# Optimization experiments

Hardware: AMD Instinct MI355X
Metric: run time of the kernel (lower is better)

The kernel has to match this reference:

```python
import jax, jax.numpy as jnp
import numpy as np

D = 1024
H = 16
DH = D // H
RATIO = 4
EPS = 1e-5


def layer_norm(x, g, b):
    mu = jnp.mean(x, axis=-1, keepdims=True)
    var = jnp.mean(jnp.square(x - mu), axis=-1, keepdims=True)
    return (x - mu) * jax.lax.rsqrt(var + EPS) * g + b


def setup_inputs() -> dict:
    key = jax.random.key(0)
    ks = jax.random.split(key, 12)
    s = 1.0 / np.sqrt(D)
    inp = {
        "x": jax.random.normal(ks[0], (4, 2048, D), dtype=jnp.float32),
        "Wq": jax.random.normal(ks[1], (D, D), dtype=jnp.float32) * s,
        "bq": jnp.zeros((D,), jnp.float32),
        "Wk": jax.random.normal(ks[2], (D, D), dtype=jnp.float32) * s,
        "bk": jnp.zeros((D,), jnp.float32),
        "Wv": jax.random.normal(ks[3], (D, D), dtype=jnp.float32) * s,
        "bv": jnp.zeros((D,), jnp.float32),
        "Wfc": jax.random.normal(ks[4], (D, D), dtype=jnp.float32) * s,
        "bfc": jnp.zeros((D,), jnp.float32),
        "ln1_g": jnp.ones((D,), jnp.float32),
        "ln1_b": jnp.zeros((D,), jnp.float32),
        "W1": jax.random.normal(ks[5], (D, D * RATIO), dtype=jnp.float32) * s,
        "b1": jnp.zeros((D * RATIO,), jnp.float32),
        "W2": jax.random.normal(ks[6], (D * RATIO, D), dtype=jnp.float32) * (1.0 / np.sqrt(D * RATIO)),
        "b2": jnp.zeros((D,), jnp.float32),
        "ln2_g": jnp.ones((D,), jnp.float32),
        "ln2_b": jnp.zeros((D,), jnp.float32),
    }
    return inp


def reference(x, Wq, bq, Wk, bk, Wv, bv, Wfc, bfc, ln1_g, ln1_b, W1, b1, W2, b2, ln2_g, ln2_b):
    B, S, _ = x.shape
    # QKV projections -> [B, H, S, DH]
    q = (x @ Wq + bq).reshape(B, S, H, DH).transpose(0, 2, 1, 3)
    k = (x @ Wk + bk).reshape(B, S, H, DH).transpose(0, 2, 1, 3)
    v = (x @ Wv + bv).reshape(B, S, H, DH).transpose(0, 2, 1, 3)
    scores = jnp.einsum("bhqd,bhkd->bhqk", q, k) / np.sqrt(DH)
    w = jax.nn.softmax(scores, axis=-1)
    attn = jnp.einsum("bhqk,bhkd->bhqd", w, v)
    attn = attn.transpose(0, 2, 1, 3).reshape(B, S, D)
    attn_out = attn @ Wfc + bfc  # dropout = identity (droprate=0)
    h = layer_norm(x + attn_out, ln1_g, ln1_b)
    m = jax.nn.relu(h @ W1 + b1)
    m = m @ W2 + b2
    # NOTE: original code applies mlp_norm without residual
    return layer_norm(m, ln2_g, ln2_b)
```

## Files before the change

### kernel.cpp

```cpp
#include <hip/hip_runtime.h>
#include <hip/hip_bf16.h>

#define DEV __device__ __forceinline__

typedef __attribute__((ext_vector_type(8))) short short8;
typedef __attribute__((ext_vector_type(4))) float f32x4;

DEV f32x4 mfma16(short8 a, short8 b, f32x4 c) {
  return __builtin_amdgcn_mfma_f32_16x16x32_bf16(a, b, c, 0, 0, 0);
}

DEV unsigned short f2bf(float f) {
  union { float f; unsigned u; } x; x.f = f;
  unsigned r = x.u + 0x7fffu + ((x.u >> 16) & 1u);
  return (unsigned short)(r >> 16);
}

__global__ __launch_bounds__(256) void cvt_bf16(const float* __restrict__ in,
                                                unsigned short* __restrict__ out,
                                                int n4) {
  int i = blockIdx.x * 256 + threadIdx.x;
  if (i >= n4) return;
  float4 v = ((const float4*)in)[i];
  ushort4 o;
  o.x = f2bf(v.x); o.y = f2bf(v.y); o.z = f2bf(v.z); o.w = f2bf(v.w);
  ((ushort4*)out)[i] = o;
}

__global__ __launch_bounds__(256) void cvtT(const float* __restrict__ W,
                                            unsigned short* __restrict__ Wt,
                                            int K, int N) {
  __shared__ float t[32][33];
  int n0 = blockIdx.x * 32, k0 = blockIdx.y * 32;
  int tx = threadIdx.x, ty = threadIdx.y;
#pragma unroll
  for (int i = 0; i < 4; i++)
    t[ty * 4 + i][tx] = W[(size_t)(k0 + ty * 4 + i) * N + n0 + tx];
  __syncthreads();
#pragma unroll
  for (int i = 0; i < 4; i++)
    Wt[(size_t)(n0 + ty * 4 + i) * K + k0 + tx] = f2bf(t[tx][ty * 4 + i]);
}

enum { M_Q = 0, M_K = 1, M_V = 2, M_RES = 3, M_RELU = 4, M_F32 = 5 };

template <int MODE>
__global__ __launch_bounds__(256, 2)
void gemm_bt(const unsigned short* __restrict__ A,
             const unsigned short* __restrict__ Bt,
             const float* __restrict__ bias,
             const float* __restrict__ res,
             void* __restrict__ outp, int M, int N, int K) {
  __shared__ unsigned short lA[128 * 64];
  __shared__ unsigned short lB[128 * 64];
  const int tid = threadIdx.x;
  const int l = tid & 63, w = tid >> 6;
  const int wr = w >> 1, wc = w & 1;
  const int lr = l & 15, lg = l >> 4;
  const int m0 = blockIdx.x * 128, n0 = blockIdx.y * 128;
  f32x4 acc[4][4] = {};

  for (int k0 = 0; k0 < K; k0 += 64) {
    __syncthreads();
#pragma unroll
    for (int i = 0; i < 4; i++) {
      int off = (i * 256 + tid) * 8;
      int r = off >> 6, c = off & 63;
      __builtin_amdgcn_global_load_lds(
          (const __attribute__((address_space(1))) unsigned int*)(A + (size_t)(m0 + r) * K + k0 + c),
          (__attribute__((address_space(3))) unsigned int*)(lA + off), 16, 0, 0);
    }
#pragma unroll
    for (int i = 0; i < 4; i++) {
      int off = (i * 256 + tid) * 8;
      int r = off >> 6, c = off & 63;
      __builtin_amdgcn_global_load_lds(
          (const __attribute__((address_space(1))) unsigned int*)(Bt + (size_t)(n0 + r) * K + k0 + c),
          (__attribute__((address_space(3))) unsigned int*)(lB + off), 16, 0, 0);
    }
    __syncthreads();
#pragma unroll
    for (int kk = 0; kk < 2; kk++) {
      short8 af[4], bfr[4];
#pragma unroll
      for (int mt = 0; mt < 4; mt++)
        af[mt] = *(const short8*)(lA + (wr * 64 + mt * 16 + lr) * 64 + kk * 32 + lg * 8);
#pragma unroll
      for (int nt = 0; nt < 4; nt++)
        bfr[nt] = *(const short8*)(lB + (wc * 64 + nt * 16 + lr) * 64 + kk * 32 + lg * 8);
#pragma unroll
      for (int mt = 0; mt < 4; mt++)
#pragma unroll
        for (int nt = 0; nt < 4; nt++)
          acc[mt][nt] = mfma16(af[mt], bfr[nt], acc[mt][nt]);
    }
  }

#pragma unroll
  for (int mt = 0; mt < 4; mt++) {
#pragma unroll
    for (int nt = 0; nt < 4; nt++) {
#pragma unroll
      for (int r = 0; r < 4; r++) {
        int row = m0 + wr * 64 + mt * 16 + lg * 4 + r;
        int col = n0 + wc * 64 + nt * 16 + lr;
        float v = acc[mt][nt][r] + bias[col];
        if constexpr (MODE == M_Q || MODE == M_K || MODE == M_V) {
          int b = row >> 11, s = row & 2047;
          int h = col >> 6, dh = col & 63;
          if constexpr (MODE == M_Q) {
            ((unsigned short*)outp)[(((size_t)(b * 16 + h) * 2048 + s) << 6) + dh] = f2bf(v * 0.125f);
          } else if constexpr (MODE == M_K) {
            ((unsigned short*)outp)[(((size_t)(b * 16 + h) * 2048 + s) << 6) + dh] = f2bf(v);
          } else {
            ((unsigned short*)outp)[((size_t)(b * 16 + h) * 64 + dh) * 2048 + s] = f2bf(v);
          }
        } else if constexpr (MODE == M_RES) {
          size_t idx = (size_t)row * N + col;
          ((float*)outp)[idx] = v + res[idx];
        } else if constexpr (MODE == M_RELU) {
          ((unsigned short*)outp)[(size_t)row * N + col] = f2bf(v > 0.f ? v : 0.f);
        } else {
          ((float*)outp)[(size_t)row * N + col] = v;
        }
      }
    }
  }
}

__global__ __launch_bounds__(256, 2)
void flash_attn(const unsigned short* __restrict__ Q,
                const unsigned short* __restrict__ Kb,
                const unsigned short* __restrict__ Vt,
                unsigned short* __restrict__ attnb) {
  const int S = 2048;
  __shared__ unsigned short Qs[64 * 64], Ks[64 * 64], Vs[64 * 64];
  __shared__ unsigned short Ps[4][16 * 64];
  const int tid = threadIdx.x, l = tid & 63, w = tid >> 6;
  const int lr = l & 15, lg = l >> 4;
  const int bh = blockIdx.y, q0 = blockIdx.x * 64;
  const unsigned short* Qp = Q + (size_t)bh * S * 64;
  const unsigned short* Kp = Kb + (size_t)bh * S * 64;
  const unsigned short* Vp = Vt + (size_t)bh * 64 * S;

#pragma unroll
  for (int i = 0; i < 2; i++) {
    int off = (i * 256 + tid) * 8;
    int r = off >> 6, c = off & 63;
    *(short8*)((char*)Qs + r * 128 + ((c * 2) ^ ((r & 7) << 4))) =
        *(const short8*)(Qp + (size_t)(q0 + r) * 64 + c);
  }
  __syncthreads();
  short8 qf[2];
#pragma unroll
  for (int kk = 0; kk < 2; kk++) {
    int rq = w * 16 + lr;
    qf[kk] = *(const short8*)((char*)Qs + rq * 128 + (((kk * 32 + lg * 8) * 2) ^ ((rq & 7) << 4)));
  }

  float m_run[4], l_run[4];
  f32x4 oacc[4] = {};
#pragma unroll
  for (int r = 0; r < 4; r++) { m_run[r] = -1e30f; l_run[r] = 0.f; }

  for (int kv0 = 0; kv0 < S; kv0 += 64) {
    __syncthreads();
#pragma unroll
    for (int i = 0; i < 2; i++) {
      int off = (i * 256 + tid) * 8;
      int r = off >> 6, c = off & 63;
      *(short8*)((char*)Ks + r * 128 + ((c * 2) ^ ((r & 7) << 4))) =
          *(const short8*)(Kp + (size_t)(kv0 + r) * 64 + c);
      *(short8*)((char*)Vs + r * 128 + ((c * 2) ^ ((r & 7) << 4))) =
          *(const short8*)(Vp + (size_t)r * S + kv0 + c);
    }
    __syncthreads();

    f32x4 sa[4] = {};
#pragma unroll
    for (int nt = 0; nt < 4; nt++) {
#pragma unroll
      for (int kk = 0; kk < 2; kk++) {
        int rk = nt * 16 + lr;
        short8 kf = *(const short8*)((char*)Ks + rk * 128 + (((kk * 32 + lg * 8) * 2) ^ ((rk & 7) << 4)));
        sa[nt] = mfma16(qf[kk], kf, sa[nt]);
      }
    }

    float tmax[4], p[4][4], tsum[4];
#pragma unroll
    for (int r = 0; r < 4; r++)
      tmax[r] = fmaxf(fmaxf(sa[0][r], sa[1][r]), fmaxf(sa[2][r], sa[3][r]));
#pragma unroll
    for (int d = 1; d < 16; d <<= 1)
#pragma unroll
      for (int r = 0; r < 4; r++) tmax[r] = fmaxf(tmax[r], __shfl_xor(tmax[r], d, 64));
#pragma unroll
    for (int r = 0; r < 4; r++) {
      float mnew = fmaxf(m_run[r], tmax[r]);
      float corr = __expf(m_run[r] - mnew);
      tsum[r] = 0.f;
#pragma unroll
      for (int nt = 0; nt < 4; nt++) { p[nt][r] = __expf(sa[nt][r] - mnew); tsum[r] += p[nt][r]; }
      m_run[r] = mnew;
      l_run[r] *= corr;
#pragma unroll
      for (int nt = 0; nt < 4; nt++) oacc[nt][r] *= corr;
    }
#pragma unroll
    for (int d = 1; d < 16; d <<= 1)
#pragma unroll
      for (int r = 0; r < 4; r++) tsum[r] += __shfl_xor(tsum[r], d, 64);
#pragma unroll
    for (int r = 0; r < 4; r++) l_run[r] += tsum[r];

    unsigned short* Pw = Ps[w];
#pragma unroll
    for (int nt = 0; nt < 4; nt++)
#pragma unroll
      for (int r = 0; r < 4; r++) {
        int rr = lg * 4 + r;
        *(unsigned short*)((char*)Pw + rr * 128 + (((nt * 16 + lr) * 2) ^ ((rr & 7) << 4))) = f2bf(p[nt][r]);
      }
#pragma unroll
    for (int kk = 0; kk < 2; kk++) {
      short8 pf = *(const short8*)((char*)Pw + lr * 128 + (((kk * 32 + lg * 8) * 2) ^ ((lr & 7) << 4)));
#pragma unroll
      for (int nt = 0; nt < 4; nt++) {
        int rv = nt * 16 + lr;
        short8 vf = *(const short8*)((char*)Vs + rv * 128 + (((kk * 32 + lg * 8) * 2) ^ ((rv & 7) << 4)));
        oacc[nt] = mfma16(pf, vf, oacc[nt]);
      }
    }
  }

  const int b = bh >> 4, h = bh & 15;
#pragma unroll
  for (int nt = 0; nt < 4; nt++)
#pragma unroll
    for (int r = 0; r < 4; r++) {
      int s = q0 + w * 16 + lg * 4 + r;
      int col = h * 64 + nt * 16 + lr;
      attnb[(size_t)(b * 2048 + s) * 1024 + col] = f2bf(oacc[nt][r] / l_run[r]);
    }
}

template <int OUTF32>
__global__ __launch_bounds__(256)
void ln_row(const float* __restrict__ in, const float* __restrict__ g,
            const float* __restrict__ b, void* __restrict__ outp) {
  const int row = blockIdx.x, tid = threadIdx.x;
  float4 v = ((const float4*)(in + (size_t)row * 1024))[tid];
  float s = v.x + v.y + v.z + v.w;
  float s2 = v.x * v.x + v.y * v.y + v.z * v.z + v.w * v.w;
#pragma unroll
  for (int d = 1; d < 64; d <<= 1) { s += __shfl_xor(s, d, 64); s2 += __shfl_xor(s2, d, 64); }
  __shared__ float ps[8];
  if ((tid & 63) == 0) { ps[tid >> 6] = s; ps[4 + (tid >> 6)] = s2; }
  __syncthreads();
  s = ps[0] + ps[1] + ps[2] + ps[3];
  s2 = ps[4] + ps[5] + ps[6] + ps[7];
  float mu = s * (1.f / 1024.f);
  float var = s2 * (1.f / 1024.f) - mu * mu;
  float rstd = rsqrtf(var + 1e-5f);
  float4 gv = ((const float4*)g)[tid];
  float4 bv = ((const float4*)b)[tid];
  float o0 = (v.x - mu) * rstd * gv.x + bv.x;
  float o1 = (v.y - mu) * rstd * gv.y + bv.y;
  float o2 = (v.z - mu) * rstd * gv.z + bv.z;
  float o3 = (v.w - mu) * rstd * gv.w + bv.w;
  if constexpr (OUTF32) {
    float4 o; o.x = o0; o.y = o1; o.z = o2; o.w = o3;
    ((float4*)outp)[(size_t)row * 256 + tid] = o;
  } else {
    ushort4 o; o.x = f2bf(o0); o.y = f2bf(o1); o.z = f2bf(o2); o.w = f2bf(o3);
    ((ushort4*)outp)[(size_t)row * 256 + tid] = o;
  }
}

extern "C" void kernel_launch(void* const* d_in, const int* in_sizes, int n_in,
                              void* d_out, int out_size, void* d_ws, size_t ws_size,
                              hipStream_t stream) {
  const float* x   = (const float*)d_in[0];
  const float* Wq  = (const float*)d_in[1];
  const float* bq  = (const float*)d_in[2];
  const float* Wk  = (const float*)d_in[3];
  const float* bk  = (const float*)d_in[4];
  const float* Wv  = (const float*)d_in[5];
  const float* bv  = (const float*)d_in[6];
  const float* Wfc = (const float*)d_in[7];
  const float* bfc = (const float*)d_in[8];
  const float* g1  = (const float*)d_in[9];
  const float* bn1 = (const float*)d_in[10];
  const float* W1  = (const float*)d_in[11];
  const float* b1  = (const float*)d_in[12];
  const float* W2  = (const float*)d_in[13];
  const float* b2  = (const float*)d_in[14];
  const float* g2  = (const float*)d_in[15];
  const float* bn2 = (const float*)d_in[16];

  char* ws = (char*)d_ws;
  size_t off = 0;
  auto alloc = [&](size_t bytes) { size_t o = off; off += (bytes + 255) & ~(size_t)255; return o; };
  unsigned short* xb  = (unsigned short*)(ws + alloc(8192UL * 1024 * 2));
  unsigned short* Wqt = (unsigned short*)(ws + alloc(1024UL * 1024 * 2));
  unsigned short* Wkt = (unsigned short*)(ws + alloc(1024UL * 1024 * 2));
  unsigned short* Wvt = (unsigned short*)(ws + alloc(1024UL * 1024 * 2));
  unsigned short* Wft = (unsigned short*)(ws + alloc(1024UL * 1024 * 2));
  unsigned short* W1t = (unsigned short*)(ws + alloc(4096UL * 1024 * 2));
  unsigned short* W2t = (unsigned short*)(ws + alloc(1024UL * 4096 * 2));
  char* zoneA = ws + alloc(67108864UL);
  float* y    = (float*)(ws + alloc(33554432UL));
  unsigned short* hb = (unsigned short*)(ws + alloc(16777216UL));

  unsigned short* Qb    = (unsigned short*)zoneA;
  unsigned short* Kbuf  = Qb + 8388608;
  unsigned short* Vtb   = Kbuf + 8388608;
  unsigned short* attnb = Vtb + 8388608;
  unsigned short* mb    = (unsigned short*)zoneA;
  float* m2 = y;

  dim3 tb(32, 8);
  cvt_bf16<<<8192, 256, 0, stream>>>(x, xb, 2097152);
  cvtT<<<dim3(32, 32), tb, 0, stream>>>(Wq, Wqt, 1024, 1024);
  cvtT<<<dim3(32, 32), tb, 0, stream>>>(Wk, Wkt, 1024, 1024);
  cvtT<<<dim3(32, 32), tb, 0, stream>>>(Wv, Wvt, 1024, 1024);
  cvtT<<<dim3(32, 32), tb, 0, stream>>>(Wfc, Wft, 1024, 1024);
  cvtT<<<dim3(128, 32), tb, 0, stream>>>(W1, W1t, 1024, 4096);
  cvtT<<<dim3(32, 128), tb, 0, stream>>>(W2, W2t, 4096, 1024);

  gemm_bt<M_Q><<<dim3(64, 8), 256, 0, stream>>>(xb, Wqt, bq, nullptr, Qb, 8192, 1024, 1024);
  gemm_bt<M_K><<<dim3(64, 8), 256, 0, stream>>>(xb, Wkt, bk, nullptr, Kbuf, 8192, 1024, 1024);
  gemm_bt<M_V><<<dim3(64, 8), 256, 0, stream>>>(xb, Wvt, bv, nullptr, Vtb, 8192, 1024, 1024);

  flash_attn<<<dim3(32, 64), 256, 0, stream>>>(Qb, Kbuf, Vtb, attnb);

  gemm_bt<M_RES><<<dim3(64, 8), 256, 0, stream>>>(attnb, Wft, bfc, x, y, 8192, 1024, 1024);
  ln_row<0><<<8192, 256, 0, stream>>>(y, g1, bn1, hb);
  gemm_bt<M_RELU><<<dim3(64, 32), 256, 0, stream>>>(hb, W1t, b1, nullptr, mb, 8192, 4096, 1024);
  gemm_bt<M_F32><<<dim3(64, 8), 256, 0, stream>>>(mb, W2t, b2, nullptr, m2, 8192, 1024, 4096);
  ln_row<1><<<8192, 256, 0, stream>>>(m2, g2, bn2, d_out);
}
```

Baseline: 686.7 us.

## Double-buffer K/V tiles in flash attention with direct global-to-LDS loads

Flash attention now keeps two K and two V buffers in LDS and prefetches the next tile with global_load_lds while computing on the current one, which removes one barrier per iteration and the register round trip for staging. The P scratch reuses the Q tile's LDS, since Q is held in registers after the initial read, and launch bounds rise to 4 blocks per CU. The goal is to overlap global loads with MFMA and softmax work and to raise occupancy. Correctness relies on waiting for the async LDS loads (vmcnt) before the barrier, and the higher occupancy target may force register spills.

```diff
diff --git a/kernel.cpp b/kernel.cpp
--- a/kernel.cpp
+++ b/kernel.cpp
@@ -128,14 +128,15 @@
   }
 }
 
-__global__ __launch_bounds__(256, 2)
+__global__ __launch_bounds__(256, 4)
 void flash_attn(const unsigned short* __restrict__ Q,
                 const unsigned short* __restrict__ Kb,
                 const unsigned short* __restrict__ Vt,
                 unsigned short* __restrict__ attnb) {
   const int S = 2048;
-  __shared__ unsigned short Qs[64 * 64], Ks[64 * 64], Vs[64 * 64];
-  __shared__ unsigned short Ps[4][16 * 64];
+  __shared__ unsigned short Qs[64 * 64];
+  __shared__ unsigned short Ks[2][64 * 64];
+  __shared__ unsigned short Vs[2][64 * 64];
   const int tid = threadIdx.x, l = tid & 63, w = tid >> 6;
   const int lr = l & 15, lg = l >> 4;
   const int bh = blockIdx.y, q0 = blockIdx.x * 64;
@@ -143,38 +144,44 @@
   const unsigned short* Kp = Kb + (size_t)bh * S * 64;
   const unsigned short* Vp = Vt + (size_t)bh * 64 * S;
 
-#pragma unroll
-  for (int i = 0; i < 2; i++) {
-    int off = (i * 256 + tid) * 8;
-    int r = off >> 6, c = off & 63;
-    *(short8*)((char*)Qs + r * 128 + ((c * 2) ^ ((r & 7) << 4))) =
-        *(const short8*)(Qp + (size_t)(q0 + r) * 64 + c);
-  }
+  auto stage64 = [&](const unsigned short* gbase, size_t rstride, unsigned short* lds) {
+#pragma unroll
+    for (int i = 0; i < 2; i++) {
+      int off16 = i * 256 + tid;
+      int r = off16 >> 3;
+      int chs = (off16 & 7) ^ (r & 7);
+      __builtin_amdgcn_global_load_lds(
+          (const __attribute__((address_space(1))) unsigned int*)(gbase + (size_t)r * rstride + chs * 8),
+          (__attribute__((address_space(3))) unsigned int*)(lds + (size_t)off16 * 8), 16, 0, 0);
+    }
+  };
+
+  stage64(Qp + (size_t)q0 * 64, 64, Qs);
+  stage64(Kp, 64, Ks[0]);
+  stage64(Vp, S, Vs[0]);
   __syncthreads();
+
   short8 qf[2];
 #pragma unroll
   for (int kk = 0; kk < 2; kk++) {
     int rq = w * 16 + lr;
     qf[kk] = *(const short8*)((char*)Qs + rq * 128 + (((kk * 32 + lg * 8) * 2) ^ ((rq & 7) << 4)));
   }
+  unsigned short* Pw = Qs + w * 1024;
 
   float m_run[4], l_run[4];
   f32x4 oacc[4] = {};
 #pragma unroll
   for (int r = 0; r < 4; r++) { m_run[r] = -1e30f; l_run[r] = 0.f; }
 
+  int cur = 0;
   for (int kv0 = 0; kv0 < S; kv0 += 64) {
-    __syncthreads();
-#pragma unroll
-    for (int i = 0; i < 2; i++) {
-      int off = (i * 256 + tid) * 8;
-      int r = off >> 6, c = off & 63;
-      *(short8*)((char*)Ks + r * 128 + ((c * 2) ^ ((r & 7) << 4))) =
-          *(const short8*)(Kp + (size_t)(kv0 + r) * 64 + c);
-      *(short8*)((char*)Vs + r * 128 + ((c * 2) ^ ((r & 7) << 4))) =
-          *(const short8*)(Vp + (size_t)r * S + kv0 + c);
-    }
-    __syncthreads();
+    if (kv0 + 64 < S) {
+      stage64(Kp + (size_t)(kv0 + 64) * 64, 64, Ks[cur ^ 1]);
+      stage64(Vp + (kv0 + 64), S, Vs[cur ^ 1]);
+    }
+    const unsigned short* Kc = Ks[cur];
+    const unsigned short* Vc = Vs[cur];
 
     f32x4 sa[4] = {};
 #pragma unroll
@@ -182,7 +189,7 @@
 #pragma unroll
       for (int kk = 0; kk < 2; kk++) {
         int rk = nt * 16 + lr;
-        short8 kf = *(const short8*)((char*)Ks + rk * 128 + (((kk * 32 + lg * 8) * 2) ^ ((rk & 7) << 4)));
+        short8 kf = *(const short8*)((const char*)Kc + rk * 128 + (((kk * 32 + lg * 8) * 2) ^ ((rk & 7) << 4)));
         sa[nt] = mfma16(qf[kk], kf, sa[nt]);
       }
     }
@@ -214,7 +221,6 @@
 #pragma unroll
     for (int r = 0; r < 4; r++) l_run[r] += tsum[r];
 
-    unsigned short* Pw = Ps[w];
 #pragma unroll
     for (int nt = 0; nt < 4; nt++)
 #pragma unroll
@@ -228,10 +234,13 @@
 #pragma unroll
       for (int nt = 0; nt < 4; nt++) {
         int rv = nt * 16 + lr;
-        short8 vf = *(const short8*)((char*)Vs + rv * 128 + (((kk * 32 + lg * 8) * 2) ^ ((rv & 7) << 4)));
+        short8 vf = *(const short8*)((const char*)Vc + rv * 128 + (((kk * 32 + lg * 8) * 2) ^ ((rv & 7) << 4)));
         oacc[nt] = mfma16(pf, vf, oacc[nt]);
       }
     }
+
+    __syncthreads();
+    cur ^= 1;
   }
 
   const int b = bh >> 4, h = bh & 15;
```

After: 673.5 us. Within noise of the previous version (-1.9%).
